# Performance work log

Measured on AMD Instinct MI355X. Metric: run time of the kernel, lower is better.

The kernel has to match this reference:

```python
import jax, jax.numpy as jnp
import numpy as np

D_MODEL = 768
N_HEADS = 12
HEAD_DIM = D_MODEL // N_HEADS


def setup_inputs() -> dict:
    key = jax.random.key(0)
    ks = jax.random.split(key, 7)
    B, S = 4, 2048
    scale = 1.0 / np.sqrt(D_MODEL)
    return {
        "hidden_states": jax.random.normal(ks[0], (B, S, D_MODEL), dtype=jnp.float32),
        "attention_mask": jnp.ones((B, S), dtype=jnp.float32),
        "Wq": jax.random.normal(ks[1], (D_MODEL, D_MODEL), dtype=jnp.float32) * scale,
        "bq": jnp.zeros((D_MODEL,), dtype=jnp.float32),
        "Wk": jax.random.normal(ks[2], (D_MODEL, D_MODEL), dtype=jnp.float32) * scale,
        "bk": jnp.zeros((D_MODEL,), dtype=jnp.float32),
        "Wv": jax.random.normal(ks[3], (D_MODEL, D_MODEL), dtype=jnp.float32) * scale,
        "bv": jnp.zeros((D_MODEL,), dtype=jnp.float32),
    }


def reference(hidden_states, attention_mask, Wq, bq, Wk, bk, Wv, bv):
    B, S, _ = hidden_states.shape

    def heads(x):  # [B,S,D] -> [B,H,S,hd]
        return x.reshape(B, S, N_HEADS, HEAD_DIM).transpose(0, 2, 1, 3)

    q = heads(hidden_states @ Wq + bq)
    k = heads(hidden_states @ Wk + bk)
    v = heads(hidden_states @ Wv + bv)

    # [B,H,S,S] scores -- explicitly materialized, as in the original module
    scores = jnp.einsum("bhqd,bhkd->bhqk", q, k) / np.sqrt(HEAD_DIM)
    mask_add = (1.0 - attention_mask)[:, None, None, :] * -10000.0
    scores = scores + mask_add
    probs = jax.nn.softmax(scores, axis=-1)  # dropout p=0 (eval) -> identity

    ctx = jnp.einsum("bhqk,bhkd->bhqd", probs, v)
    ctx = ctx.transpose(0, 2, 1, 3).reshape(B, S, D_MODEL)
    return ctx, probs
```

## Files before the change

kernel.cpp:

```cpp
#include <hip/hip_runtime.h>
#include <hip/hip_bf16.h>
#include <cstdint>

typedef short bf16x8 __attribute__((ext_vector_type(8)));
typedef float f32x4 __attribute__((ext_vector_type(4)));
typedef unsigned short ushort_t;

__device__ __forceinline__ ushort_t f2bf(float f) {
    uint32_t u = __float_as_uint(f);
    u = (u + 0x7fffu + ((u >> 16) & 1u)) >> 16;
    return (ushort_t)u;
}

__device__ __forceinline__ ushort_t f2bf_native(float f) {
    __hip_bfloat16 h = __float2bfloat16(f);
    return *reinterpret_cast<ushort_t*>(&h);
}

__device__ __forceinline__ void gl2lds16(const void* g, void* l) {
    __builtin_amdgcn_global_load_lds((const __attribute__((address_space(1))) void*)(g),
                                     (__attribute__((address_space(3))) void*)(l), 16, 0, 0);
}

__device__ __forceinline__ void wait_vm0() {
    asm volatile("s_waitcnt vmcnt(0)" ::: "memory");
}
__device__ __forceinline__ void wait_vm8() {
    asm volatile("s_waitcnt vmcnt(8)" ::: "memory");
}

__global__ void cvt_hidden(const float* __restrict__ in, ushort_t* __restrict__ out, int n4) {
    int i = blockIdx.x * blockDim.x + threadIdx.x;
    for (; i < n4; i += gridDim.x * blockDim.x) {
        float4 v = ((const float4*)in)[i];
        ushort_t tmp[4] __attribute__((aligned(8)));
        tmp[0] = f2bf(v.x); tmp[1] = f2bf(v.y); tmp[2] = f2bf(v.z); tmp[3] = f2bf(v.w);
        ((uint2*)out)[i] = *(uint2*)tmp;
    }
}

__global__ void wt_transpose(const float* __restrict__ Wq, const float* __restrict__ Wk,
                             const float* __restrict__ Wv, ushort_t* __restrict__ out) {
    __shared__ float tile[64][68];
    const float* W = blockIdx.z == 0 ? Wq : (blockIdx.z == 1 ? Wk : Wv);
    int k0 = blockIdx.x * 64, n0 = blockIdx.y * 64;
    int t = threadIdx.x;
    for (int i = 0; i < 4; ++i) {
        int e = i * 1024 + t * 4;
        int r = e >> 6, c = e & 63;
        float4 v = *(const float4*)(W + (k0 + r) * 768 + n0 + c);
        *(float4*)(&tile[r][c]) = v;
    }
    __syncthreads();
    ushort_t* o = out + blockIdx.z * 768 * 768;
    for (int i = 0; i < 2; ++i) {
        int e = i * 2048 + t * 8;
        int rn = e >> 6, ck = e & 63;
        ushort_t tmp[8] __attribute__((aligned(16)));
        for (int j = 0; j < 8; ++j) tmp[j] = f2bf(tile[ck + j][rn]);
        *(int4*)(o + (n0 + rn) * 768 + k0 + ck) = *(int4*)tmp;
    }
}

__launch_bounds__(256, 2)
__global__ void qkv_gemm(const ushort_t* __restrict__ A, const ushort_t* __restrict__ Wt,
                         const float* __restrict__ bq, const float* __restrict__ bk,
                         const float* __restrict__ bv,
                         ushort_t* __restrict__ q_out, ushort_t* __restrict__ k_out,
                         ushort_t* __restrict__ vt_out) {
    __shared__ char smem[32768];
    char* sA = smem;
    char* sB = smem + 16384;
    int z = blockIdx.z;
    const ushort_t* Wz = Wt + z * 589824;
    const float* bias = z == 0 ? bq : (z == 1 ? bk : bv);
    int m0 = blockIdx.x * 128, n0 = blockIdx.y * 128;
    int t = threadIdx.x, lane = t & 63, w = t >> 6;
    int wr = w >> 1, wc = w & 1;
    int lr = lane & 15, lg = lane >> 4;
    f32x4 acc[4][4] = {};
    for (int kt = 0; kt < 768; kt += 64) {
        for (int i = 0; i < 4; ++i) {
            int e = i * 2048 + t * 8;
            int r = e >> 6, c = e & 63;
            bf16x8 va = *(const bf16x8*)(A + (m0 + r) * 768 + kt + c);
            *(bf16x8*)(sA + ((r * 128 + c * 2) ^ ((r & 7) << 4))) = va;
            bf16x8 vb = *(const bf16x8*)(Wz + (n0 + r) * 768 + kt + c);
            *(bf16x8*)(sB + ((r * 128 + c * 2) ^ ((r & 7) << 4))) = vb;
        }
        __syncthreads();
        bf16x8 af[2][4], bfr[2][4];
#pragma unroll
        for (int kf = 0; kf < 2; ++kf)
#pragma unroll
            for (int mf = 0; mf < 4; ++mf) {
                int row = wr * 64 + mf * 16 + lr;
                af[kf][mf] = *(const bf16x8*)(sA + ((row * 128 + (kf * 32 + lg * 8) * 2) ^ ((row & 7) << 4)));
            }
#pragma unroll
        for (int kf = 0; kf < 2; ++kf)
#pragma unroll
            for (int nf = 0; nf < 4; ++nf) {
                int row = wc * 64 + nf * 16 + lr;
                bfr[kf][nf] = *(const bf16x8*)(sB + ((row * 128 + (kf * 32 + lg * 8) * 2) ^ ((row & 7) << 4)));
            }
#pragma unroll
        for (int kf = 0; kf < 2; ++kf)
#pragma unroll
            for (int mf = 0; mf < 4; ++mf)
#pragma unroll
                for (int nf = 0; nf < 4; ++nf)
                    acc[mf][nf] = __builtin_amdgcn_mfma_f32_16x16x32_bf16(af[kf][mf], bfr[kf][nf], acc[mf][nf], 0, 0, 0);
        __syncthreads();
    }
    if (z == 2) {
        for (int nf = 0; nf < 4; ++nf) {
            int n = n0 + wc * 64 + nf * 16 + lr;
            float bv_ = bias[n];
            int h = n >> 6, d = n & 63;
            for (int mf = 0; mf < 4; ++mf) {
                int m = m0 + wr * 64 + mf * 16 + lg * 4;
                int b = m >> 11, s = m & 2047;
                ushort_t tmp[4] __attribute__((aligned(8)));
                for (int rr = 0; rr < 4; ++rr) tmp[rr] = f2bf(acc[mf][nf][rr] + bv_);
                *(uint2*)(vt_out + ((size_t)(b * 12 + h) * 64 + d) * 2048 + s) = *(uint2*)tmp;
            }
        }
    } else {
        ushort_t* outp = z == 0 ? q_out : k_out;
        float scale = z == 0 ? 0.125f : 1.0f;
        for (int nf = 0; nf < 4; ++nf) {
            int n = n0 + wc * 64 + nf * 16 + lr;
            float bv_ = bias[n];
            int h = n >> 6, d = n & 63;
            for (int mf = 0; mf < 4; ++mf) {
                for (int rr = 0; rr < 4; ++rr) {
                    int m = m0 + wr * 64 + mf * 16 + lg * 4 + rr;
                    float val = (acc[mf][nf][rr] + bv_) * scale;
                    int b = m >> 11, s = m & 2047;
                    outp[((b * 12 + h) * 2048 + s) * 64 + d] = f2bf(val);
                }
            }
        }
    }
}

__launch_bounds__(256, 3)
__global__ void attn_fused(const ushort_t* __restrict__ qs, const ushort_t* __restrict__ ks,
                           const ushort_t* __restrict__ vt, const float* __restrict__ mask,
                           float* __restrict__ ctx, float* __restrict__ probs) {
    __shared__ char smem[49152];
    char* sK = smem;
    char* sV = smem + 16384;
    char* sP = smem + 32768;
    int qt = blockIdx.x, bh = blockIdx.y;
    int b = bh / 12, h = bh % 12;
    int q0 = qt * 128;
    int t = threadIdx.x, lane = t & 63, w = t >> 6;
    int lr = lane & 15, lg = lane >> 4;
    const ushort_t* Qb = qs + bh * 131072;
    const ushort_t* Kb = ks + bh * 131072;
    const ushort_t* Vb = vt + bh * 131072;
    const float* mb = mask + b * 2048;
    float* prow = probs + (size_t)bh * 4194304;

    int rsub = lane >> 3;
    int jsw  = ((lane & 7) ^ rsub) * 8;

#pragma unroll
    for (int i = 0; i < 4; ++i) {
        int r = i * 32 + w * 8 + rsub;
        gl2lds16(Qb + (q0 + r) * 64 + jsw, sK + i * 4096 + w * 1024);
    }
    wait_vm0();
    __syncthreads();
    bf16x8 qa[2][2];
#pragma unroll
    for (int mf = 0; mf < 2; ++mf)
#pragma unroll
        for (int kf = 0; kf < 2; ++kf) {
            int row = w * 32 + mf * 16 + lr;
            qa[mf][kf] = *(const bf16x8*)(sK + ((row * 128 + (kf * 32 + lg * 8) * 2) ^ ((row & 7) << 4)));
        }
    __syncthreads();

#pragma unroll
    for (int t2 = 0; t2 < 2; ++t2)
#pragma unroll
        for (int i = 0; i < 2; ++i) {
            int r = t2 * 64 + i * 32 + w * 8 + rsub;
            gl2lds16(Kb + r * 64 + jsw, smem + t2 * 8192 + i * 4096 + w * 1024);
        }
    wait_vm0();
    __syncthreads();
    float lsum[2] = {0.f, 0.f};
    int cur = 0;
    for (int kp = 0; kp < 16; ++kp) {
        char* bufc = smem + cur * 16384;
        if (kp < 15) {
            char* bufn = smem + (cur ^ 1) * 16384;
#pragma unroll
            for (int t2 = 0; t2 < 2; ++t2)
#pragma unroll
                for (int i = 0; i < 2; ++i) {
                    int r = ((kp + 1) * 2 + t2) * 64 + i * 32 + w * 8 + rsub;
                    gl2lds16(Kb + r * 64 + jsw, bufn + t2 * 8192 + i * 4096 + w * 1024);
                }
        }
#pragma unroll
        for (int t2 = 0; t2 < 2; ++t2) {
            int kt = kp * 2 + t2;
            char* sKc = bufc + t2 * 8192;
#pragma unroll
            for (int n16 = 0; n16 < 4; ++n16) {
                int krow = n16 * 16 + lr;
                bf16x8 kb0 = *(const bf16x8*)(sKc + ((krow * 128 + (lg * 8) * 2) ^ ((krow & 7) << 4)));
                bf16x8 kb1 = *(const bf16x8*)(sKc + ((krow * 128 + (32 + lg * 8) * 2) ^ ((krow & 7) << 4)));
                float4 m4 = *(const float4*)(mb + kt * 64 + n16 * 16 + lg * 4);
                float ma0 = (1.0f - m4.x) * -10000.0f;
                float ma1 = (1.0f - m4.y) * -10000.0f;
                float ma2 = (1.0f - m4.z) * -10000.0f;
                float ma3 = (1.0f - m4.w) * -10000.0f;
#pragma unroll
                for (int mf = 0; mf < 2; ++mf) {
                    f32x4 sacc = {};
                    sacc = __builtin_amdgcn_mfma_f32_16x16x32_bf16(kb0, qa[mf][0], sacc, 0, 0, 0);
                    sacc = __builtin_amdgcn_mfma_f32_16x16x32_bf16(kb1, qa[mf][1], sacc, 0, 0, 0);
                    lsum[mf] += (__expf(sacc[0] + ma0) + __expf(sacc[1] + ma1))
                              + (__expf(sacc[2] + ma2) + __expf(sacc[3] + ma3));
                }
            }
        }
        wait_vm0();
        __syncthreads();
        cur ^= 1;
    }
#pragma unroll
    for (int mf = 0; mf < 2; ++mf) {
        lsum[mf] += __shfl_xor(lsum[mf], 16);
        lsum[mf] += __shfl_xor(lsum[mf], 32);
    }
    float inv2[2] = {1.0f / lsum[0], 1.0f / lsum[1]};

#pragma unroll
    for (int i = 0; i < 2; ++i) {
        int r = i * 32 + w * 8 + rsub;
        gl2lds16(Kb + r * 64 + jsw, sK + i * 4096 + w * 1024);
        gl2lds16(Vb + r * 2048 + jsw, sV + i * 4096 + w * 1024);
    }
    wait_vm0();
    __syncthreads();

    f32x4 oacc[2][4] = {};
    cur = 0;
    for (int kt = 0; kt < 32; ++kt) {
        char* sKc = sK + cur * 8192;
        char* sVc = sV + cur * 8192;
        if (kt < 31) {
            char* sKn = sK + (cur ^ 1) * 8192;
            char* sVn = sV + (cur ^ 1) * 8192;
            int nt = kt + 1;
#pragma unroll
            for (int i = 0; i < 2; ++i) {
                int r = i * 32 + w * 8 + rsub;
                gl2lds16(Kb + (nt * 64 + r) * 64 + jsw, sKn + i * 4096 + w * 1024);
                gl2lds16(Vb + r * 2048 + nt * 64 + jsw, sVn + i * 4096 + w * 1024);
            }
        }
#pragma unroll
        for (int n16 = 0; n16 < 4; ++n16) {
            int krow = n16 * 16 + lr;
            bf16x8 kb0 = *(const bf16x8*)(sKc + ((krow * 128 + (lg * 8) * 2) ^ ((krow & 7) << 4)));
            bf16x8 kb1 = *(const bf16x8*)(sKc + ((krow * 128 + (32 + lg * 8) * 2) ^ ((krow & 7) << 4)));
            float4 m4 = *(const float4*)(mb + kt * 64 + n16 * 16 + lg * 4);
            float ma0 = (1.0f - m4.x) * -10000.0f;
            float ma1 = (1.0f - m4.y) * -10000.0f;
            float ma2 = (1.0f - m4.z) * -10000.0f;
            float ma3 = (1.0f - m4.w) * -10000.0f;
#pragma unroll
            for (int mf = 0; mf < 2; ++mf) {
                f32x4 sacc = {};
                sacc = __builtin_amdgcn_mfma_f32_16x16x32_bf16(kb0, qa[mf][0], sacc, 0, 0, 0);
                sacc = __builtin_amdgcn_mfma_f32_16x16x32_bf16(kb1, qa[mf][1], sacc, 0, 0, 0);
                ushort_t tmp[4] __attribute__((aligned(8)));
                tmp[0] = f2bf_native(__expf(sacc[0] + ma0) * inv2[mf]);
                tmp[1] = f2bf_native(__expf(sacc[1] + ma1) * inv2[mf]);
                tmp[2] = f2bf_native(__expf(sacc[2] + ma2) * inv2[mf]);
                tmp[3] = f2bf_native(__expf(sacc[3] + ma3) * inv2[mf]);
                *(uint2*)(sP + w * 4096 + mf * 2048 +
                          ((lr * 128 + n16 * 32 + lg * 8) ^ ((lr & 7) << 4))) = *(uint2*)tmp;
            }
        }
#pragma unroll
        for (int mf = 0; mf < 2; ++mf)
#pragma unroll
            for (int step = 0; step < 4; ++step) {
                int srow = step * 4 + lg;
                uint2 uu = *(const uint2*)(sP + w * 4096 + mf * 2048 +
                                           ((srow * 128 + lr * 8) ^ ((srow & 7) << 4)));
                f32x4 pv;
                pv[0] = __uint_as_float((uu.x & 0xffffu) << 16);
                pv[1] = __uint_as_float(uu.x & 0xffff0000u);
                pv[2] = __uint_as_float((uu.y & 0xffffu) << 16);
                pv[3] = __uint_as_float(uu.y & 0xffff0000u);
                *(f32x4*)(prow + (size_t)(q0 + w * 32 + mf * 16 + srow) * 2048 + kt * 64 + lr * 4) = pv;
            }
        __builtin_amdgcn_s_setprio(1);
#pragma unroll
        for (int mf = 0; mf < 2; ++mf)
#pragma unroll
            for (int kf = 0; kf < 2; ++kf) {
                bf16x8 pa = *(const bf16x8*)(sP + w * 4096 + mf * 2048 +
                                             ((lr * 128 + (kf * 32 + lg * 8) * 2) ^ ((lr & 7) << 4)));
#pragma unroll
                for (int dt = 0; dt < 4; ++dt) {
                    int vrow = dt * 16 + lr;
                    bf16x8 vb = *(const bf16x8*)(sVc + ((vrow * 128 + (kf * 32 + lg * 8) * 2) ^ ((vrow & 7) << 4)));
                    oacc[mf][dt] = __builtin_amdgcn_mfma_f32_16x16x32_bf16(pa, vb, oacc[mf][dt], 0, 0, 0);
                }
            }
        __builtin_amdgcn_s_setprio(0);
        wait_vm8();
        __syncthreads();
        cur ^= 1;
    }
#pragma unroll
    for (int mf = 0; mf < 2; ++mf)
#pragma unroll
        for (int dt = 0; dt < 4; ++dt)
#pragma unroll
            for (int r = 0; r < 4; ++r) {
                int qabs = q0 + w * 32 + mf * 16 + lg * 4 + r;
                ctx[(size_t)(b * 2048 + qabs) * 768 + h * 64 + dt * 16 + lr] = oacc[mf][dt][r];
            }
}

extern "C" void kernel_launch(void* const* d_in, const int* in_sizes, int n_in,
                              void* d_out, int out_size, void* d_ws, size_t ws_size,
                              hipStream_t stream) {
    const float* hidden = (const float*)d_in[0];
    const float* mask   = (const float*)d_in[1];
    const float* Wq     = (const float*)d_in[2];
    const float* bq     = (const float*)d_in[3];
    const float* Wk     = (const float*)d_in[4];
    const float* bk     = (const float*)d_in[5];
    const float* Wv     = (const float*)d_in[6];
    const float* bv     = (const float*)d_in[7];
    float* ctx   = (float*)d_out;
    float* probs = ctx + 6291456;

    char* ws = (char*)d_ws;
    ushort_t* hidB = (ushort_t*)(ws);
    ushort_t* WtB  = (ushort_t*)(ws + 12582912);
    ushort_t* qsB  = (ushort_t*)(ws + 16121856);
    ushort_t* ksB  = (ushort_t*)(ws + 28704768);
    ushort_t* vtB  = (ushort_t*)(ws + 41287680);

    hipLaunchKernelGGL(cvt_hidden, dim3(6144), dim3(256), 0, stream, hidden, hidB, 1572864);
    hipLaunchKernelGGL(wt_transpose, dim3(12, 12, 3), dim3(256), 0, stream, Wq, Wk, Wv, WtB);
    hipLaunchKernelGGL(qkv_gemm, dim3(64, 6, 3), dim3(256), 0, stream,
                       hidB, WtB, bq, bk, bv, qsB, ksB, vtB);
    hipLaunchKernelGGL(attn_fused, dim3(16, 48), dim3(256), 0, stream, qsB, ksB, vtB, mask, ctx, probs);
}
```

Baseline: 272.2 us.

## Double-buffer QKV GEMM with async global-to-LDS loads and remap attention blocks

The QKV GEMM now double-buffers its A and W tiles in 64KB of LDS. It issues global_load_lds for the next k-tile while running MFMAs on the current one and raises wave priority around the MFMA block. This is meant to hide global load latency that was previously exposed behind a sync every iteration. The attention launch becomes 1D, with a block-id permutation that spreads the heads across XCDs for better L2 locality. Doubling LDS to 64KB may cut GEMM occupancy below the 2 blocks per CU that the launch bounds request.

```diff
diff --git a/kernel.cpp b/kernel.cpp
--- a/kernel.cpp
+++ b/kernel.cpp
@@ -68,9 +68,9 @@
                          const float* __restrict__ bv,
                          ushort_t* __restrict__ q_out, ushort_t* __restrict__ k_out,
                          ushort_t* __restrict__ vt_out) {
-    __shared__ char smem[32768];
+    __shared__ char smem[65536];
     char* sA = smem;
-    char* sB = smem + 16384;
+    char* sB = smem + 32768;
     int z = blockIdx.z;
     const ushort_t* Wz = Wt + z * 589824;
     const float* bias = z == 0 ? bq : (z == 1 ? bk : bv);
@@ -78,32 +78,50 @@
     int t = threadIdx.x, lane = t & 63, w = t >> 6;
     int wr = w >> 1, wc = w & 1;
     int lr = lane & 15, lg = lane >> 4;
+    int rsub = lane >> 3;
+    int jsw  = ((lane & 7) ^ rsub) * 8;
+
+#pragma unroll
+    for (int i = 0; i < 4; ++i) {
+        int r = i * 32 + w * 8 + rsub;
+        gl2lds16(A + (m0 + r) * 768 + jsw, sA + i * 4096 + w * 1024);
+        gl2lds16(Wz + (n0 + r) * 768 + jsw, sB + i * 4096 + w * 1024);
+    }
+    wait_vm0();
+    __syncthreads();
+
     f32x4 acc[4][4] = {};
-    for (int kt = 0; kt < 768; kt += 64) {
-        for (int i = 0; i < 4; ++i) {
-            int e = i * 2048 + t * 8;
-            int r = e >> 6, c = e & 63;
-            bf16x8 va = *(const bf16x8*)(A + (m0 + r) * 768 + kt + c);
-            *(bf16x8*)(sA + ((r * 128 + c * 2) ^ ((r & 7) << 4))) = va;
-            bf16x8 vb = *(const bf16x8*)(Wz + (n0 + r) * 768 + kt + c);
-            *(bf16x8*)(sB + ((r * 128 + c * 2) ^ ((r & 7) << 4))) = vb;
-        }
-        __syncthreads();
+    int cur = 0;
+    for (int ktile = 0; ktile < 12; ++ktile) {
+        char* sAc = sA + cur * 16384;
+        char* sBc = sB + cur * 16384;
+        if (ktile < 11) {
+            char* sAn = sA + (cur ^ 1) * 16384;
+            char* sBn = sB + (cur ^ 1) * 16384;
+            int kt = (ktile + 1) * 64;
+#pragma unroll
+            for (int i = 0; i < 4; ++i) {
+                int r = i * 32 + w * 8 + rsub;
+                gl2lds16(A + (m0 + r) * 768 + kt + jsw, sAn + i * 4096 + w * 1024);
+                gl2lds16(Wz + (n0 + r) * 768 + kt + jsw, sBn + i * 4096 + w * 1024);
+            }
+        }
         bf16x8 af[2][4], bfr[2][4];
 #pragma unroll
         for (int kf = 0; kf < 2; ++kf)
 #pragma unroll
             for (int mf = 0; mf < 4; ++mf) {
                 int row = wr * 64 + mf * 16 + lr;
-                af[kf][mf] = *(const bf16x8*)(sA + ((row * 128 + (kf * 32 + lg * 8) * 2) ^ ((row & 7) << 4)));
+                af[kf][mf] = *(const bf16x8*)(sAc + ((row * 128 + (kf * 32 + lg * 8) * 2) ^ ((row & 7) << 4)));
             }
 #pragma unroll
         for (int kf = 0; kf < 2; ++kf)
 #pragma unroll
             for (int nf = 0; nf < 4; ++nf) {
                 int row = wc * 64 + nf * 16 + lr;
-                bfr[kf][nf] = *(const bf16x8*)(sB + ((row * 128 + (kf * 32 + lg * 8) * 2) ^ ((row & 7) << 4)));
-            }
+                bfr[kf][nf] = *(const bf16x8*)(sBc + ((row * 128 + (kf * 32 + lg * 8) * 2) ^ ((row & 7) << 4)));
+            }
+        __builtin_amdgcn_s_setprio(1);
 #pragma unroll
         for (int kf = 0; kf < 2; ++kf)
 #pragma unroll
@@ -111,7 +129,10 @@
 #pragma unroll
                 for (int nf = 0; nf < 4; ++nf)
                     acc[mf][nf] = __builtin_amdgcn_mfma_f32_16x16x32_bf16(af[kf][mf], bfr[kf][nf], acc[mf][nf], 0, 0, 0);
+        __builtin_amdgcn_s_setprio(0);
+        wait_vm0();
         __syncthreads();
+        cur ^= 1;
     }
     if (z == 2) {
         for (int nf = 0; nf < 4; ++nf) {
@@ -153,7 +174,9 @@
     char* sK = smem;
     char* sV = smem + 16384;
     char* sP = smem + 32768;
-    int qt = blockIdx.x, bh = blockIdx.y;
+    int id = blockIdx.x;
+    int nid = (id & 7) * 96 + (id >> 3);
+    int qt = nid & 15, bh = nid >> 4;
     int b = bh / 12, h = bh % 12;
     int q0 = qt * 128;
     int t = threadIdx.x, lane = t & 63, w = t >> 6;
@@ -360,5 +383,5 @@
     hipLaunchKernelGGL(wt_transpose, dim3(12, 12, 3), dim3(256), 0, stream, Wq, Wk, Wv, WtB);
     hipLaunchKernelGGL(qkv_gemm, dim3(64, 6, 3), dim3(256), 0, stream,
                        hidB, WtB, bq, bk, bv, qsB, ksB, vtB);
-    hipLaunchKernelGGL(attn_fused, dim3(16, 48), dim3(256), 0, stream, qsB, ksB, vtB, mask, ctx, probs);
-}
+    hipLaunchKernelGGL(attn_fused, dim3(768), dim3(256), 0, stream, qsB, ksB, vtB, mask, ctx, probs);
+}
```

Result: faster. 265.6 us (-2.4%).
